# Performance work log

Measured on AMD Instinct MI355X. Metric: run time of the kernel, lower is better.

## Reference

```python
import jax, jax.numpy as jnp
import numpy as np

N_NODES = 50000
N_EDGES = 800000
N_GRAPHS = 64
IN_CH = 128
HID_G = 256
HID_FC = 256
OUT_CH = 128


def setup_inputs() -> dict:
    key = jax.random.key(0)
    ks = jax.random.split(key, 16)
    x = jax.random.normal(ks[0], (N_NODES, IN_CH), dtype=jnp.float32)
    edge_index = jax.random.randint(ks[1], (2, N_EDGES), 0, N_NODES, dtype=jnp.int64)
    batch = jnp.sort(jax.random.randint(ks[2], (N_NODES,), 0, N_GRAPHS, dtype=jnp.int64))
    hlr = jax.random.normal(ks[3], (N_GRAPHS, 1), dtype=jnp.float32)
    std = jax.random.normal(ks[4], (N_GRAPHS, 1), dtype=jnp.float32)
    s = 0.05
    W0 = jax.random.normal(ks[5], (IN_CH, HID_G), dtype=jnp.float32) * s
    b0 = jnp.zeros((HID_G,), jnp.float32)
    W1 = jax.random.normal(ks[6], (HID_G, HID_G), dtype=jnp.float32) * s
    b1 = jnp.zeros((HID_G,), jnp.float32)
    W2 = jax.random.normal(ks[7], (HID_G, HID_G), dtype=jnp.float32) * s
    b2 = jnp.zeros((HID_G,), jnp.float32)
    fcW0 = jax.random.normal(ks[8], (HID_G + 2, HID_FC), dtype=jnp.float32) * s
    fcb0 = jnp.zeros((HID_FC,), jnp.float32)
    fcW1 = jax.random.normal(ks[9], (HID_FC, OUT_CH), dtype=jnp.float32) * s
    fcb1 = jnp.zeros((OUT_CH,), jnp.float32)
    return dict(x=x, edge_index=edge_index, batch=batch, hlr=hlr, std=std,
                W0=W0, b0=b0, W1=W1, b1=b1, W2=W2, b2=b2,
                fcW0=fcW0, fcb0=fcb0, fcW1=fcW1, fcb1=fcb1)


def _gcn_conv(h, W, b, src, dst, dis):
    # GCNConv with added self-loops and symmetric normalization:
    # out_i = sum_{j->i} d_j^{-1/2} d_i^{-1/2} (h_j W) + d_i^{-1} (h_i W) + b
    hW = h @ W  # [N, F]
    norm = dis[src] * dis[dst]  # [E]
    agg = jax.ops.segment_sum(hW[src] * norm[:, None], dst, num_segments=N_NODES)
    agg = agg + hW * (dis * dis)[:, None]  # self-loop contribution
    return agg + b


def reference(x, edge_index, batch, hlr, std, W0, b0, W1, b1, W2, b2, fcW0, fcb0, fcW1, fcb1):
    src, dst = edge_index[0], edge_index[1]
    # degree on A + I (edge weight 1), computed at destination nodes
    deg = jax.ops.segment_sum(jnp.ones((N_EDGES,), x.dtype), dst, num_segments=N_NODES) + 1.0
    dis = jax.lax.rsqrt(deg)
    h = jax.nn.relu(_gcn_conv(x, W0, b0, src, dst, dis))
    h = jax.nn.relu(_gcn_conv(h, W1, b1, src, dst, dis))
    h = jax.nn.relu(_gcn_conv(h, W2, b2, src, dst, dis))
    # global mean pool over graphs
    counts = jax.ops.segment_sum(jnp.ones((N_NODES,), x.dtype), batch, num_segments=N_GRAPHS)
    pooled = jax.ops.segment_sum(h, batch, num_segments=N_GRAPHS) / jnp.maximum(counts, 1.0)[:, None]
    z = jnp.concatenate([pooled, hlr, std], axis=1)  # [G, HID_G + 2]
    z = jax.nn.relu(z @ fcW0 + fcb0)
    return z @ fcW1 + fcb1
```

## Files before the change

### kernel.cpp

```cpp
#include <hip/hip_runtime.h>

#define NNODES 50000
#define NEDGES 800000
#define NGRAPHS 64
#define INCH 128
#define HID 256
#define ZSTR (HID + 2)
#define SCAN_B 512
#define SCAN_NB ((NNODES + SCAN_B - 1) / SCAN_B)
#define NSLICE 16
#define FILL_PASSES 2
#define PASS_NODES ((NNODES + FILL_PASSES - 1) / FILL_PASSES)

typedef __attribute__((ext_vector_type(8))) short short8v;
typedef __attribute__((ext_vector_type(8))) unsigned short ushort8v;
typedef __attribute__((ext_vector_type(4))) float f32x4;

__device__ inline ushort f2b(float f) {
    union { float f; unsigned u; } v; v.f = f;
    unsigned r = (v.u + 0x7FFFu + ((v.u >> 16) & 1u)) >> 16;
    return (ushort)r;
}
__device__ inline float b2f(ushort b) {
    union { unsigned u; float f; } v; v.u = ((unsigned)b) << 16;
    return v.f;
}

__global__ __launch_bounds__(256) void fill_pre(const int* __restrict__ dst, int* __restrict__ deg,
                                                int* __restrict__ pwn) {
    int e = blockIdx.x * 256 + threadIdx.x;
    if (e < NEDGES) pwn[e] = atomicAdd(&deg[dst[e]], 1);
}

__global__ __launch_bounds__(256) void dis_kernel(const int* __restrict__ deg, float* __restrict__ dis) {
    int i = blockIdx.x * 256 + threadIdx.x;
    if (i < NNODES) dis[i] = rsqrtf((float)deg[i] + 1.0f);
}

__global__ __launch_bounds__(SCAN_B) void scan1(const int* __restrict__ deg, int* __restrict__ row_ptr,
                                                int* __restrict__ bsum) {
    __shared__ int s[SCAN_B];
    int t = threadIdx.x;
    int i = blockIdx.x * SCAN_B + t;
    int v = (i < NNODES) ? deg[i] : 0;
    s[t] = v;
    __syncthreads();
    for (int off = 1; off < SCAN_B; off <<= 1) {
        int x = (t >= off) ? s[t - off] : 0;
        __syncthreads();
        if (t >= off) s[t] += x;
        __syncthreads();
    }
    if (i < NNODES) row_ptr[i + 1] = s[t];
    if (t == SCAN_B - 1) bsum[blockIdx.x] = s[t];
}

__global__ __launch_bounds__(128) void scan2(int* __restrict__ bsum) {
    __shared__ int s[128];
    int t = threadIdx.x;
    int v = (t < SCAN_NB) ? bsum[t] : 0;
    s[t] = v;
    __syncthreads();
    for (int off = 1; off < 128; off <<= 1) {
        int x = (t >= off) ? s[t - off] : 0;
        __syncthreads();
        if (t >= off) s[t] += x;
        __syncthreads();
    }
    if (t < SCAN_NB) bsum[t] = s[t];
}

__global__ __launch_bounds__(SCAN_B) void scan3(int* __restrict__ row_ptr, const int* __restrict__ bsum) {
    int b = blockIdx.x, t = threadIdx.x;
    int i = b * SCAN_B + t;
    if (i == 0) row_ptr[0] = 0;
    if (i < NNODES && b > 0) row_ptr[i + 1] += bsum[b - 1];
}

__global__ __launch_bounds__(256) void fill_scatter(const int* __restrict__ src, const int* __restrict__ dst,
                                                    const int* __restrict__ pwn, const int* __restrict__ row_ptr,
                                                    int* __restrict__ csr_src, int lo) {
    int e = blockIdx.x * 256 + threadIdx.x;
    if (e >= NEDGES) return;
    int d = dst[e];
    if (d < lo || d >= lo + PASS_NODES) return;
    csr_src[row_ptr[d] + pwn[e]] = src[e];
}

__global__ __launch_bounds__(256) void xcvt(const float4* __restrict__ x, const float* __restrict__ dis,
                                            ushort4* __restrict__ xb, int n4) {
    int i = blockIdx.x * 256 + threadIdx.x;
    if (i >= n4) return;
    float d = dis[i >> 5];
    float4 v = x[i];
    ushort4 o;
    o.x = f2b(d * v.x); o.y = f2b(d * v.y); o.z = f2b(d * v.z); o.w = f2b(d * v.w);
    xb[i] = o;
}

__global__ __launch_bounds__(256) void wcvt(const float* __restrict__ W, ushort* __restrict__ Wt, int K, int N) {
    int i = blockIdx.x * 256 + threadIdx.x;
    if (i >= K * N) return;
    int k = i / N, n = i - k * N;
    Wt[n * K + k] = f2b(W[i]);
}

template <int K>
__global__ __launch_bounds__(256, 5) void gcn_fused(const ushort* __restrict__ hin,
                                                    const int* __restrict__ row_ptr,
                                                    const int* __restrict__ csr_src,
                                                    const ushort* __restrict__ Bt,
                                                    const float* __restrict__ bias,
                                                    const float* __restrict__ dis,
                                                    ushort* __restrict__ hout, int scale_out) {
    __shared__ ushort As[64 * K];
    const int tid = threadIdx.x;
    const int w = tid >> 6, l = tid & 63;
    const int R0 = blockIdx.x * 64;

    constexpr int CHL = K / 8;
    constexpr int NPW = 64 / CHL;
    const int sub = l / CHL;
    const int lane = l - sub * CHL;
    const ushort* hp = hin + lane * 8;
#pragma unroll
    for (int it = 0; it < 64 / (4 * NPW); ++it) {
        int nloc = (it * 4 + w) * NPW + sub;
        int node = R0 + nloc;
        ushort8v o;
        if (node < NNODES) {
            ushort8v sv = *(const ushort8v*)&hp[(size_t)node * K];
            float a0 = b2f(sv[0]), a1 = b2f(sv[1]), a2 = b2f(sv[2]), a3 = b2f(sv[3]);
            float a4 = b2f(sv[4]), a5 = b2f(sv[5]), a6 = b2f(sv[6]), a7 = b2f(sv[7]);
            int e = row_ptr[node], e1 = row_ptr[node + 1];
            for (; e + 7 < e1; e += 8) {
                ushort8v v[8];
#pragma unroll
                for (int u = 0; u < 8; ++u) v[u] = *(const ushort8v*)&hp[(size_t)csr_src[e + u] * K];
#pragma unroll
                for (int u = 0; u < 8; ++u) {
                    a0 += b2f(v[u][0]); a1 += b2f(v[u][1]); a2 += b2f(v[u][2]); a3 += b2f(v[u][3]);
                    a4 += b2f(v[u][4]); a5 += b2f(v[u][5]); a6 += b2f(v[u][6]); a7 += b2f(v[u][7]);
                }
            }
            for (; e < e1; ++e) {
                ushort8v v0 = *(const ushort8v*)&hp[(size_t)csr_src[e] * K];
                a0 += b2f(v0[0]); a1 += b2f(v0[1]); a2 += b2f(v0[2]); a3 += b2f(v0[3]);
                a4 += b2f(v0[4]); a5 += b2f(v0[5]); a6 += b2f(v0[6]); a7 += b2f(v0[7]);
            }
            o[0] = f2b(a0); o[1] = f2b(a1); o[2] = f2b(a2); o[3] = f2b(a3);
            o[4] = f2b(a4); o[5] = f2b(a5); o[6] = f2b(a6); o[7] = f2b(a7);
        } else {
            o = ushort8v{0, 0, 0, 0, 0, 0, 0, 0};
        }
        *(ushort8v*)&As[nloc * K + ((lane * 8) ^ ((nloc & 7) * 8))] = o;
    }
    __syncthreads();

    const int r16 = l & 15, kg = l >> 4;
    f32x4 acc[4][4] = {};
#pragma unroll
    for (int k0 = 0; k0 < K; k0 += 32) {
        int k = k0 + kg * 8;
        short8v a[4], b[4];
#pragma unroll
        for (int m = 0; m < 4; ++m) {
            int row = m * 16 + r16;
            a[m] = *(const short8v*)&As[row * K + (k ^ ((row & 7) * 8))];
        }
#pragma unroll
        for (int n = 0; n < 4; ++n)
            b[n] = *(const short8v*)&Bt[(size_t)(w * 64 + n * 16 + r16) * K + k];
#pragma unroll
        for (int m = 0; m < 4; ++m)
#pragma unroll
            for (int n = 0; n < 4; ++n)
                acc[m][n] = __builtin_amdgcn_mfma_f32_16x16x32_bf16(a[m], b[n], acc[m][n], 0, 0, 0);
    }
    float bv[4];
#pragma unroll
    for (int n = 0; n < 4; ++n) bv[n] = bias[w * 64 + n * 16 + r16];
#pragma unroll
    for (int m = 0; m < 4; ++m) {
#pragma unroll
        for (int j = 0; j < 4; ++j) {
            int row = R0 + m * 16 + kg * 4 + j;
            if (row >= NNODES) continue;
            float dr = dis[row];
            float os = scale_out ? dr : 1.0f;
#pragma unroll
            for (int n = 0; n < 4; ++n) {
                float v = fmaxf(dr * acc[m][n][j] + bv[n], 0.f) * os;
                hout[(size_t)row * HID + w * 64 + n * 16 + r16] = f2b(v);
            }
        }
    }
}

__global__ __launch_bounds__(256) void graph_bounds(const int* __restrict__ batch, int* __restrict__ gstart) {
    int i = blockIdx.x * 256 + threadIdx.x;
    if (i >= NNODES) return;
    int b = batch[i];
    if (i == 0) {
        for (int g = 0; g <= b; ++g) gstart[g] = 0;
    } else {
        int pb = batch[i - 1];
        for (int g = pb + 1; g <= b; ++g) gstart[g] = i;
    }
    if (i == NNODES - 1) {
        for (int g = b + 1; g <= NGRAPHS; ++g) gstart[g] = NNODES;
    }
}

__global__ __launch_bounds__(HID) void pool_partial(const ushort* __restrict__ h, const int* __restrict__ gstart,
                                                    float* __restrict__ z) {
    int g = blockIdx.x;
    int s = blockIdx.y;
    int t = threadIdx.x;
    int n0 = gstart[g], n1 = gstart[g + 1];
    int cnt = n1 - n0;
    if (cnt <= 0) return;
    int len = (cnt + NSLICE - 1) / NSLICE;
    int a = n0 + s * len;
    int b = a + len < n1 ? a + len : n1;
    if (a >= b) return;
    float acc = 0.f;
    for (int n = a; n < b; ++n) acc += b2f(h[(size_t)n * HID + t]);
    atomicAdd(&z[g * ZSTR + t], acc);
}

__global__ __launch_bounds__(HID) void pool_finalize(const int* __restrict__ gstart, const float* __restrict__ hlr,
                                                     const float* __restrict__ stdv, float* __restrict__ z) {
    int g = blockIdx.x;
    int t = threadIdx.x;
    int cnt = gstart[g + 1] - gstart[g];
    float inv = 1.f / (float)(cnt > 0 ? cnt : 1);
    z[g * ZSTR + t] *= inv;
    if (t == 0) {
        z[g * ZSTR + HID] = hlr[g];
        z[g * ZSTR + HID + 1] = stdv[g];
    }
}

__global__ __launch_bounds__(HID) void fc_k(const float* __restrict__ z, const float* __restrict__ fcW0,
                                            const float* __restrict__ fcb0, const float* __restrict__ fcW1,
                                            const float* __restrict__ fcb1, float* __restrict__ out) {
    __shared__ float zs[ZSTR];
    __shared__ float z2[HID];
    int g = blockIdx.x;
    int t = threadIdx.x;
    zs[t] = z[g * ZSTR + t];
    if (t < 2) zs[HID + t] = z[g * ZSTR + HID + t];
    __syncthreads();
    float acc = fcb0[t];
    for (int k = 0; k < ZSTR; ++k) acc += zs[k] * fcW0[k * HID + t];
    z2[t] = fmaxf(acc, 0.f);
    __syncthreads();
    if (t < INCH) {
        float acc2 = fcb1[t];
        for (int k = 0; k < HID; ++k) acc2 += z2[k] * fcW1[k * INCH + t];
        out[g * INCH + t] = acc2;
    }
}

extern "C" void kernel_launch(void* const* d_in, const int* in_sizes, int n_in,
                              void* d_out, int out_size, void* d_ws, size_t ws_size,
                              hipStream_t stream) {
    const float* x = (const float*)d_in[0];
    const int* ei = (const int*)d_in[1];
    const int* src = ei;
    const int* dst = ei + NEDGES;
    const int* batch = (const int*)d_in[2];
    const float* hlr = (const float*)d_in[3];
    const float* stdv = (const float*)d_in[4];
    const float* W0 = (const float*)d_in[5];
    const float* b0 = (const float*)d_in[6];
    const float* W1 = (const float*)d_in[7];
    const float* b1 = (const float*)d_in[8];
    const float* W2 = (const float*)d_in[9];
    const float* b2 = (const float*)d_in[10];
    const float* fcW0 = (const float*)d_in[11];
    const float* fcb0 = (const float*)d_in[12];
    const float* fcW1 = (const float*)d_in[13];
    const float* fcb1 = (const float*)d_in[14];
    float* out = (float*)d_out;

    char* p = (char*)d_ws;
    auto alloc = [&](size_t bytes) -> char* {
        char* r = p;
        p += (bytes + 255) & ~(size_t)255;
        return r;
    };
    ushort* xb = (ushort*)alloc(sizeof(ushort) * (size_t)NNODES * INCH);
    ushort* h = (ushort*)alloc(sizeof(ushort) * (size_t)NNODES * HID);
    ushort* hb = (ushort*)alloc(sizeof(ushort) * (size_t)NNODES * HID);
    ushort* Wt0 = (ushort*)alloc(sizeof(ushort) * HID * INCH);
    ushort* Wt1 = (ushort*)alloc(sizeof(ushort) * HID * HID);
    ushort* Wt2 = (ushort*)alloc(sizeof(ushort) * HID * HID);
    float* dis = (float*)alloc(sizeof(float) * NNODES);
    int* deg = (int*)alloc(sizeof(int) * NNODES);
    int* row_ptr = (int*)alloc(sizeof(int) * (NNODES + 1));
    int* pwn = (int*)alloc(sizeof(int) * NEDGES);
    int* csr_src = (int*)alloc(sizeof(int) * NEDGES);
    int* bsum = (int*)alloc(sizeof(int) * 128);
    int* gstart = (int*)alloc(sizeof(int) * (NGRAPHS + 1));
    float* z = (float*)alloc(sizeof(float) * NGRAPHS * ZSTR);
    (void)ws_size; (void)in_sizes; (void)n_in; (void)out_size;

    const int eblocks = (NEDGES + 255) / 256;

    hipMemsetAsync(deg, 0, sizeof(int) * NNODES, stream);
    fill_pre<<<eblocks, 256, 0, stream>>>(dst, deg, pwn);
    dis_kernel<<<(NNODES + 255) / 256, 256, 0, stream>>>(deg, dis);
    scan1<<<SCAN_NB, SCAN_B, 0, stream>>>(deg, row_ptr, bsum);
    scan2<<<1, 128, 0, stream>>>(bsum);
    scan3<<<SCAN_NB, SCAN_B, 0, stream>>>(row_ptr, bsum);
    for (int pass = 0; pass < FILL_PASSES; ++pass)
        fill_scatter<<<eblocks, 256, 0, stream>>>(src, dst, pwn, row_ptr, csr_src, pass * PASS_NODES);

    xcvt<<<(NNODES * INCH / 4 + 255) / 256, 256, 0, stream>>>((const float4*)x, dis, (ushort4*)xb,
                                                              NNODES * INCH / 4);
    wcvt<<<(INCH * HID + 255) / 256, 256, 0, stream>>>(W0, Wt0, INCH, HID);
    wcvt<<<(HID * HID + 255) / 256, 256, 0, stream>>>(W1, Wt1, HID, HID);
    wcvt<<<(HID * HID + 255) / 256, 256, 0, stream>>>(W2, Wt2, HID, HID);

    const int gblocks = (NNODES + 63) / 64;
    gcn_fused<INCH><<<gblocks, 256, 0, stream>>>(xb, row_ptr, csr_src, Wt0, b0, dis, h, 1);
    gcn_fused<HID><<<gblocks, 256, 0, stream>>>(h, row_ptr, csr_src, Wt1, b1, dis, hb, 1);
    gcn_fused<HID><<<gblocks, 256, 0, stream>>>(hb, row_ptr, csr_src, Wt2, b2, dis, h, 0);

    graph_bounds<<<(NNODES + 255) / 256, 256, 0, stream>>>(batch, gstart);
    hipMemsetAsync(z, 0, sizeof(float) * NGRAPHS * ZSTR, stream);
    dim3 pgrid(NGRAPHS, NSLICE);
    pool_partial<<<pgrid, HID, 0, stream>>>(h, gstart, z);
    pool_finalize<<<NGRAPHS, HID, 0, stream>>>(gstart, hlr, stdv, z);
    fc_k<<<NGRAPHS, HID, 0, stream>>>(z, fcW0, fcb0, fcW1, fcb1, out);
}
```

Baseline: 359.5 us.

## Aggregate directly into MFMA A-operand registers, dropping the shared-memory staging tile

The fused GCN layer kernel now has each lane gather the neighbor rows for the exact node and k-slice it will feed to the MFMA A operand. The aggregated values are converted to bf16 in registers and multiplied right away, so the LDS tile and the __syncthreads are gone. Each wave now computes a 16-row by 256-column output using 16 accumulators, and every wave reads the whole Bt matrix instead of a quarter of it. The aim is to remove LDS traffic, the barrier and the occupancy limit from the 64xK shared tile. The costs are higher register pressure (NC*8 float accumulators plus 16 f32x4 accumulators), fewer edges unrolled per gather iteration (2 instead of 8), and about four times more global or L2 reads of the weights.

```diff
diff --git a/kernel.cpp b/kernel.cpp
--- a/kernel.cpp
+++ b/kernel.cpp
@@ -106,93 +106,94 @@
 }
 
 template <int K>
-__global__ __launch_bounds__(256, 5) void gcn_fused(const ushort* __restrict__ hin,
-                                                    const int* __restrict__ row_ptr,
-                                                    const int* __restrict__ csr_src,
-                                                    const ushort* __restrict__ Bt,
-                                                    const float* __restrict__ bias,
-                                                    const float* __restrict__ dis,
-                                                    ushort* __restrict__ hout, int scale_out) {
-    __shared__ ushort As[64 * K];
+__global__ __launch_bounds__(256) void gcn_reg(const ushort* __restrict__ hin,
+                                               const int* __restrict__ row_ptr,
+                                               const int* __restrict__ csr_src,
+                                               const ushort* __restrict__ Bt,
+                                               const float* __restrict__ bias,
+                                               const float* __restrict__ dis,
+                                               ushort* __restrict__ hout, int scale_out) {
+    constexpr int NC = K / 32;
     const int tid = threadIdx.x;
     const int w = tid >> 6, l = tid & 63;
-    const int R0 = blockIdx.x * 64;
-
-    constexpr int CHL = K / 8;
-    constexpr int NPW = 64 / CHL;
-    const int sub = l / CHL;
-    const int lane = l - sub * CHL;
-    const ushort* hp = hin + lane * 8;
-#pragma unroll
-    for (int it = 0; it < 64 / (4 * NPW); ++it) {
-        int nloc = (it * 4 + w) * NPW + sub;
-        int node = R0 + nloc;
-        ushort8v o;
-        if (node < NNODES) {
-            ushort8v sv = *(const ushort8v*)&hp[(size_t)node * K];
-            float a0 = b2f(sv[0]), a1 = b2f(sv[1]), a2 = b2f(sv[2]), a3 = b2f(sv[3]);
-            float a4 = b2f(sv[4]), a5 = b2f(sv[5]), a6 = b2f(sv[6]), a7 = b2f(sv[7]);
-            int e = row_ptr[node], e1 = row_ptr[node + 1];
-            for (; e + 7 < e1; e += 8) {
-                ushort8v v[8];
-#pragma unroll
-                for (int u = 0; u < 8; ++u) v[u] = *(const ushort8v*)&hp[(size_t)csr_src[e + u] * K];
-#pragma unroll
-                for (int u = 0; u < 8; ++u) {
-                    a0 += b2f(v[u][0]); a1 += b2f(v[u][1]); a2 += b2f(v[u][2]); a3 += b2f(v[u][3]);
-                    a4 += b2f(v[u][4]); a5 += b2f(v[u][5]); a6 += b2f(v[u][6]); a7 += b2f(v[u][7]);
-                }
+    const int r16 = l & 15, kg = l >> 4;
+    const int row = blockIdx.x * 64 + w * 16 + r16;
+    const ushort* hp = hin + kg * 8;
+
+    float g[NC][8];
+#pragma unroll
+    for (int c = 0; c < NC; ++c)
+#pragma unroll
+        for (int i = 0; i < 8; ++i) g[c][i] = 0.f;
+
+    if (row < NNODES) {
+        {
+            const ushort* rp = &hp[(size_t)row * K];
+            ushort8v v[NC];
+#pragma unroll
+            for (int c = 0; c < NC; ++c) v[c] = *(const ushort8v*)&rp[c * 32];
+#pragma unroll
+            for (int c = 0; c < NC; ++c)
+#pragma unroll
+                for (int i = 0; i < 8; ++i) g[c][i] += b2f(v[c][i]);
+        }
+        int e = row_ptr[row], e1 = row_ptr[row + 1];
+        for (; e + 1 < e1; e += 2) {
+            const ushort* p0 = &hp[(size_t)csr_src[e] * K];
+            const ushort* p1 = &hp[(size_t)csr_src[e + 1] * K];
+            ushort8v v0[NC], v1[NC];
+#pragma unroll
+            for (int c = 0; c < NC; ++c) {
+                v0[c] = *(const ushort8v*)&p0[c * 32];
+                v1[c] = *(const ushort8v*)&p1[c * 32];
             }
-            for (; e < e1; ++e) {
-                ushort8v v0 = *(const ushort8v*)&hp[(size_t)csr_src[e] * K];
-                a0 += b2f(v0[0]); a1 += b2f(v0[1]); a2 += b2f(v0[2]); a3 += b2f(v0[3]);
-                a4 += b2f(v0[4]); a5 += b2f(v0[5]); a6 += b2f(v0[6]); a7 += b2f(v0[7]);
-            }
-            o[0] = f2b(a0); o[1] = f2b(a1); o[2] = f2b(a2); o[3] = f2b(a3);
-            o[4] = f2b(a4); o[5] = f2b(a5); o[6] = f2b(a6); o[7] = f2b(a7);
-        } else {
-            o = ushort8v{0, 0, 0, 0, 0, 0, 0, 0};
-        }
-        *(ushort8v*)&As[nloc * K + ((lane * 8) ^ ((nloc & 7) * 8))] = o;
-    }
-    __syncthreads();
-
-    const int r16 = l & 15, kg = l >> 4;
-    f32x4 acc[4][4] = {};
-#pragma unroll
-    for (int k0 = 0; k0 < K; k0 += 32) {
-        int k = k0 + kg * 8;
-        short8v a[4], b[4];
-#pragma unroll
-        for (int m = 0; m < 4; ++m) {
-            int row = m * 16 + r16;
-            a[m] = *(const short8v*)&As[row * K + (k ^ ((row & 7) * 8))];
-        }
-#pragma unroll
-        for (int n = 0; n < 4; ++n)
-            b[n] = *(const short8v*)&Bt[(size_t)(w * 64 + n * 16 + r16) * K + k];
-#pragma unroll
-        for (int m = 0; m < 4; ++m)
-#pragma unroll
-            for (int n = 0; n < 4; ++n)
-                acc[m][n] = __builtin_amdgcn_mfma_f32_16x16x32_bf16(a[m], b[n], acc[m][n], 0, 0, 0);
-    }
-    float bv[4];
-#pragma unroll
-    for (int n = 0; n < 4; ++n) bv[n] = bias[w * 64 + n * 16 + r16];
-#pragma unroll
-    for (int m = 0; m < 4; ++m) {
-#pragma unroll
-        for (int j = 0; j < 4; ++j) {
-            int row = R0 + m * 16 + kg * 4 + j;
-            if (row >= NNODES) continue;
-            float dr = dis[row];
-            float os = scale_out ? dr : 1.0f;
-#pragma unroll
-            for (int n = 0; n < 4; ++n) {
-                float v = fmaxf(dr * acc[m][n][j] + bv[n], 0.f) * os;
-                hout[(size_t)row * HID + w * 64 + n * 16 + r16] = f2b(v);
-            }
+#pragma unroll
+            for (int c = 0; c < NC; ++c)
+#pragma unroll
+                for (int i = 0; i < 8; ++i) g[c][i] += b2f(v0[c][i]) + b2f(v1[c][i]);
+        }
+        if (e < e1) {
+            const ushort* p0 = &hp[(size_t)csr_src[e] * K];
+            ushort8v v0[NC];
+#pragma unroll
+            for (int c = 0; c < NC; ++c) v0[c] = *(const ushort8v*)&p0[c * 32];
+#pragma unroll
+            for (int c = 0; c < NC; ++c)
+#pragma unroll
+                for (int i = 0; i < 8; ++i) g[c][i] += b2f(v0[c][i]);
+        }
+    }
+
+    short8v a[NC];
+#pragma unroll
+    for (int c = 0; c < NC; ++c)
+#pragma unroll
+        for (int i = 0; i < 8; ++i) a[c][i] = (short)f2b(g[c][i]);
+
+    f32x4 acc[16] = {};
+#pragma unroll
+    for (int c = 0; c < NC; ++c) {
+#pragma unroll
+        for (int n = 0; n < 16; ++n) {
+            short8v b = *(const short8v*)&Bt[(size_t)(n * 16 + r16) * K + c * 32 + kg * 8];
+            acc[n] = __builtin_amdgcn_mfma_f32_16x16x32_bf16(a[c], b, acc[n], 0, 0, 0);
+        }
+    }
+
+    float bv[16];
+#pragma unroll
+    for (int n = 0; n < 16; ++n) bv[n] = bias[n * 16 + r16];
+    const int row0 = blockIdx.x * 64 + w * 16 + kg * 4;
+#pragma unroll
+    for (int j = 0; j < 4; ++j) {
+        int r = row0 + j;
+        if (r >= NNODES) continue;
+        float dr = dis[r];
+        float os = scale_out ? dr : 1.0f;
+#pragma unroll
+        for (int n = 0; n < 16; ++n) {
+            float v = fmaxf(dr * acc[n][j] + bv[n], 0.f) * os;
+            hout[(size_t)r * HID + n * 16 + r16] = f2b(v);
         }
     }
 }
@@ -325,9 +326,9 @@
     wcvt<<<(HID * HID + 255) / 256, 256, 0, stream>>>(W2, Wt2, HID, HID);
 
     const int gblocks = (NNODES + 63) / 64;
-    gcn_fused<INCH><<<gblocks, 256, 0, stream>>>(xb, row_ptr, csr_src, Wt0, b0, dis, h, 1);
-    gcn_fused<HID><<<gblocks, 256, 0, stream>>>(h, row_ptr, csr_src, Wt1, b1, dis, hb, 1);
-    gcn_fused<HID><<<gblocks, 256, 0, stream>>>(hb, row_ptr, csr_src, Wt2, b2, dis, h, 0);
+    gcn_reg<INCH><<<gblocks, 256, 0, stream>>>(xb, row_ptr, csr_src, Wt0, b0, dis, h, 1);
+    gcn_reg<HID><<<gblocks, 256, 0, stream>>>(h, row_ptr, csr_src, Wt1, b1, dis, hb, 1);
+    gcn_reg<HID><<<gblocks, 256, 0, stream>>>(hb, row_ptr, csr_src, Wt2, b2, dis, h, 0);
 
     graph_bounds<<<(NNODES + 255) / 256, 256, 0, stream>>>(batch, gstart);
     hipMemsetAsync(z, 0, sizeof(float) * NGRAPHS * ZSTR, stream);
```

Result: slower. 479.8 us (+33.5%).

## Split GCN kernel into producer/consumer warps with double-buffered LDS

Applied to the files above, without the earlier changes.

Replaces the fused gather-then-MFMA kernel with a 768-thread block in which 8 producer warps gather neighbour rows for 16-node slices into a double-buffered LDS tile. Meanwhile 4 consumer warps run MFMA on the previous slice. The aim is to overlap the latency-bound sparse gather with the dense matmul inside each block. In exchange, blocks are larger, register and occupancy pressure change, and each consumer reloads B from global memory for every slice.

```diff
diff --git a/kernel.cpp b/kernel.cpp
--- a/kernel.cpp
+++ b/kernel.cpp
@@ -106,28 +106,63 @@
 }
 
 template <int K>
-__global__ __launch_bounds__(256, 5) void gcn_fused(const ushort* __restrict__ hin,
-                                                    const int* __restrict__ row_ptr,
-                                                    const int* __restrict__ csr_src,
-                                                    const ushort* __restrict__ Bt,
-                                                    const float* __restrict__ bias,
-                                                    const float* __restrict__ dis,
-                                                    ushort* __restrict__ hout, int scale_out) {
-    __shared__ ushort As[64 * K];
+__global__ __launch_bounds__(768, 6) void gcn_pc(const ushort* __restrict__ hin,
+                                                 const int* __restrict__ row_ptr,
+                                                 const int* __restrict__ csr_src,
+                                                 const ushort* __restrict__ Bt,
+                                                 const float* __restrict__ bias,
+                                                 const float* __restrict__ dis,
+                                                 ushort* __restrict__ hout, int scale_out) {
+    __shared__ ushort As[2][16 * K];
     const int tid = threadIdx.x;
     const int w = tid >> 6, l = tid & 63;
     const int R0 = blockIdx.x * 64;
-
     constexpr int CHL = K / 8;
     constexpr int NPW = 64 / CHL;
+    const bool producer = (w < 8);
+
     const int sub = l / CHL;
     const int lane = l - sub * CHL;
+    const int nl = w * NPW + sub;
     const ushort* hp = hin + lane * 8;
-#pragma unroll
-    for (int it = 0; it < 64 / (4 * NPW); ++it) {
-        int nloc = (it * 4 + w) * NPW + sub;
-        int node = R0 + nloc;
-        ushort8v o;
+
+    const int c = w - 8;
+    const int r16 = l & 15, kg = l >> 4;
+
+    auto consume = [&](int s) {
+        const ushort* asb = As[s & 1];
+        f32x4 acc[4] = {};
+#pragma unroll
+        for (int k0 = 0; k0 < K; k0 += 32) {
+            int k = k0 + kg * 8;
+            short8v a = *(const short8v*)&asb[r16 * K + (k ^ ((r16 & 7) * 8))];
+#pragma unroll
+            for (int n = 0; n < 4; ++n) {
+                short8v b = *(const short8v*)&Bt[(size_t)(c * 64 + n * 16 + r16) * K + k];
+                acc[n] = __builtin_amdgcn_mfma_f32_16x16x32_bf16(a, b, acc[n], 0, 0, 0);
+            }
+        }
+        float bv[4];
+#pragma unroll
+        for (int n = 0; n < 4; ++n) bv[n] = bias[c * 64 + n * 16 + r16];
+#pragma unroll
+        for (int j = 0; j < 4; ++j) {
+            int row = R0 + s * 16 + kg * 4 + j;
+            if (row >= NNODES) continue;
+            float dr = dis[row];
+            float os = scale_out ? dr : 1.0f;
+#pragma unroll
+            for (int n = 0; n < 4; ++n) {
+                float v = fmaxf(dr * acc[n][j] + bv[n], 0.f) * os;
+                hout[(size_t)row * HID + c * 64 + n * 16 + r16] = f2b(v);
+            }
+        }
+    };
+
+    auto produce = [&](int s) {
+        if (nl >= 16) return;
+        int node = R0 + s * 16 + nl;
+        ushort8v o = ushort8v{0, 0, 0, 0, 0, 0, 0, 0};
         if (node < NNODES) {
             ushort8v sv = *(const ushort8v*)&hp[(size_t)node * K];
             float a0 = b2f(sv[0]), a1 = b2f(sv[1]), a2 = b2f(sv[2]), a3 = b2f(sv[3]);
@@ -150,51 +185,17 @@
             }
             o[0] = f2b(a0); o[1] = f2b(a1); o[2] = f2b(a2); o[3] = f2b(a3);
             o[4] = f2b(a4); o[5] = f2b(a5); o[6] = f2b(a6); o[7] = f2b(a7);
-        } else {
-            o = ushort8v{0, 0, 0, 0, 0, 0, 0, 0};
         }
-        *(ushort8v*)&As[nloc * K + ((lane * 8) ^ ((nloc & 7) * 8))] = o;
-    }
-    __syncthreads();
-
-    const int r16 = l & 15, kg = l >> 4;
-    f32x4 acc[4][4] = {};
-#pragma unroll
-    for (int k0 = 0; k0 < K; k0 += 32) {
-        int k = k0 + kg * 8;
-        short8v a[4], b[4];
-#pragma unroll
-        for (int m = 0; m < 4; ++m) {
-            int row = m * 16 + r16;
-            a[m] = *(const short8v*)&As[row * K + (k ^ ((row & 7) * 8))];
-        }
-#pragma unroll
-        for (int n = 0; n < 4; ++n)
-            b[n] = *(const short8v*)&Bt[(size_t)(w * 64 + n * 16 + r16) * K + k];
-#pragma unroll
-        for (int m = 0; m < 4; ++m)
-#pragma unroll
-            for (int n = 0; n < 4; ++n)
-                acc[m][n] = __builtin_amdgcn_mfma_f32_16x16x32_bf16(a[m], b[n], acc[m][n], 0, 0, 0);
-    }
-    float bv[4];
-#pragma unroll
-    for (int n = 0; n < 4; ++n) bv[n] = bias[w * 64 + n * 16 + r16];
-#pragma unroll
-    for (int m = 0; m < 4; ++m) {
-#pragma unroll
-        for (int j = 0; j < 4; ++j) {
-            int row = R0 + m * 16 + kg * 4 + j;
-            if (row >= NNODES) continue;
-            float dr = dis[row];
-            float os = scale_out ? dr : 1.0f;
-#pragma unroll
-            for (int n = 0; n < 4; ++n) {
-                float v = fmaxf(dr * acc[m][n][j] + bv[n], 0.f) * os;
-                hout[(size_t)row * HID + w * 64 + n * 16 + r16] = f2b(v);
-            }
-        }
-    }
+        *(ushort8v*)&As[s & 1][nl * K + ((lane * 8) ^ ((nl & 7) * 8))] = o;
+    };
+
+#pragma unroll 1
+    for (int s = 0; s < 4; ++s) {
+        if (producer) produce(s);
+        else if (s > 0) consume(s - 1);
+        __syncthreads();
+    }
+    if (!producer) consume(3);
 }
 
 __global__ __launch_bounds__(256) void graph_bounds(const int* __restrict__ batch, int* __restrict__ gstart) {
@@ -325,9 +326,9 @@
     wcvt<<<(HID * HID + 255) / 256, 256, 0, stream>>>(W2, Wt2, HID, HID);
 
     const int gblocks = (NNODES + 63) / 64;
-    gcn_fused<INCH><<<gblocks, 256, 0, stream>>>(xb, row_ptr, csr_src, Wt0, b0, dis, h, 1);
-    gcn_fused<HID><<<gblocks, 256, 0, stream>>>(h, row_ptr, csr_src, Wt1, b1, dis, hb, 1);
-    gcn_fused<HID><<<gblocks, 256, 0, stream>>>(hb, row_ptr, csr_src, Wt2, b2, dis, h, 0);
+    gcn_pc<INCH><<<gblocks, 768, 0, stream>>>(xb, row_ptr, csr_src, Wt0, b0, dis, h, 1);
+    gcn_pc<HID><<<gblocks, 768, 0, stream>>>(h, row_ptr, csr_src, Wt1, b1, dis, hb, 1);
+    gcn_pc<HID><<<gblocks, 768, 0, stream>>>(hb, row_ptr, csr_src, Wt2, b2, dis, h, 0);
 
     graph_bounds<<<(NNODES + 255) / 256, 256, 0, stream>>>(batch, gstart);
     hipMemsetAsync(z, 0, sizeof(float) * NGRAPHS * ZSTR, stream);
```

Result: slower. 474.0 us (+31.8%).
